# Kernel tuning notes

Measured on AMD Instinct MI355X. Metric: run time of the kernel, lower is better.

## Reference

```python
import jax, jax.numpy as jnp
import numpy as np

N_NODES = 50000
N_EDGES = 800000
IN_DIM = 128
ATT_DIM = 128
NEG_SLOPE = 0.01  # nn.LeakyReLU default


def setup_inputs() -> dict:
    key = jax.random.key(0)
    ks = jax.random.split(key, 8)
    x = jax.random.normal(ks[0], (N_NODES, IN_DIM), dtype=jnp.float32)
    src_idx = jax.random.randint(ks[1], (N_EDGES,), 0, N_NODES, dtype=jnp.int32)
    dst_idx = jax.random.randint(ks[2], (N_EDGES,), 0, N_NODES, dtype=jnp.int32)
    # small init scale keeps exp(score) numerically tame
    src_w = jax.random.normal(ks[3], (IN_DIM, ATT_DIM), dtype=jnp.float32) * 0.05
    src_b = jnp.zeros((ATT_DIM,), dtype=jnp.float32)
    dst_w = jax.random.normal(ks[4], (IN_DIM, ATT_DIM), dtype=jnp.float32) * 0.05
    dst_b = jnp.zeros((ATT_DIM,), dtype=jnp.float32)
    att_w = jax.random.normal(ks[5], (ATT_DIM, 1), dtype=jnp.float32) * 0.05
    att_b = jnp.zeros((1,), dtype=jnp.float32)
    return {"x": x, "src_idx": src_idx, "dst_idx": dst_idx,
            "src_w": src_w, "src_b": src_b, "dst_w": dst_w, "dst_b": dst_b,
            "att_w": att_w, "att_b": att_b}


def reference(x, src_idx, dst_idx, src_w, src_b, dst_w, dst_b, att_w, att_b):
    n = x.shape[0]
    # 1) mean aggregation of source features onto destinations (copy_u + mean)
    deg = jax.ops.segment_sum(jnp.ones_like(dst_idx, dtype=x.dtype), dst_idx, num_segments=n)
    h_mean = jax.ops.segment_sum(x[src_idx], dst_idx, num_segments=n)
    h_mean = h_mean / jnp.maximum(deg, 1.0)[:, None]
    # 2) attention projections on nodes (dense GEMMs)
    ha_src = x @ src_w + src_b          # [N, att_dim]
    ha_dst = h_mean @ dst_w + dst_b     # [N, att_dim]
    # 3) per-edge u_add_v -> LeakyReLU -> att Linear -> exp
    e = jax.nn.leaky_relu(ha_src[src_idx] + ha_dst[dst_idx], NEG_SLOPE)  # [E, att_dim]
    s = jnp.exp(e @ att_w + att_b)      # [E, 1]
    # 4) edge softmax: normalize by segment sum over destination
    denom = jax.ops.segment_sum(s, dst_idx, num_segments=n)  # [N, 1]
    a = s / denom[dst_idx]              # [E, 1]
    # 5) u_mul_e weighted aggregation (sum)
    out = jax.ops.segment_sum(x[src_idx] * a, dst_idx, num_segments=n)  # [N, in_dim]
    return out
```

## Files before the change

### kernel.cpp

```cpp
#include <hip/hip_runtime.h>
#include <math.h>

#define N_NODES 50000
#define N_EDGES 800000
#define DIM 128
#define NEG_SLOPE 0.01f
#define CAP 64
#define DEGS 32

#define GEMM_BLOCKS ((N_NODES + 63) / 64)
#define EPB 1024

typedef short v8s __attribute__((ext_vector_type(8)));
typedef float v4f __attribute__((ext_vector_type(4)));

__device__ inline unsigned f2bf2(float a, float b) {
    unsigned ua = __float_as_uint(a);
    unsigned ub = __float_as_uint(b);
    ua = (ua + 0x7fffu + ((ua >> 16) & 1u)) >> 16;
    ub = (ub + 0x7fffu + ((ub >> 16) & 1u)) & 0xffff0000u;
    return ua | ub;
}
__device__ inline float2 bf2f(unsigned u) {
    float2 r;
    r.x = __uint_as_float(u << 16);
    r.y = __uint_as_float(u & 0xffff0000u);
    return r;
}

__device__ inline float2 pka(float2 a, float2 b) {
    return make_float2(a.x + b.x, a.y + b.y);
}
__device__ inline float2 pkfma(float2 a, float2 b, float2 c) {
    return make_float2(fmaf(a.x, b.x, c.x), fmaf(a.y, b.y, c.y));
}
__device__ inline float2 leaky2(float2 v) {
    return make_float2(fmaxf(v.x, v.x * NEG_SLOPE), fmaxf(v.y, v.y * NEG_SLOPE));
}

#define ROR_ADD(v, CTRL) \
    ((v) + __int_as_float(__builtin_amdgcn_update_dpp( \
        0, __float_as_int(v), (CTRL), 0xf, 0xf, false)))

__global__ __launch_bounds__(256) void k_prepw(
    const float* __restrict__ src_w, const float* __restrict__ dst_w,
    unsigned* __restrict__ whT, int* __restrict__ deg)
{
    int gid = blockIdx.x * 256 + threadIdx.x;
    if (gid < 256 * 64) {
        int n = gid >> 6;
        int kk = gid & 63;
        const float* W = (n < 128) ? src_w : dst_w;
        int col = n & 127;
        float w0 = W[(2 * kk) * DIM + col];
        float w1 = W[(2 * kk + 1) * DIM + col];
        whT[gid] = f2bf2(w0, w1);
    }
    if (gid < N_NODES) deg[gid * DEGS] = 0;
}

__global__ __launch_bounds__(256) void k_scatgemm(
    const int* __restrict__ src, const int* __restrict__ dst,
    int* __restrict__ deg, int* __restrict__ slots,
    const float* __restrict__ x, const unsigned* __restrict__ whT,
    const float* __restrict__ src_b, unsigned* __restrict__ hx_u,
    unsigned* __restrict__ yu)
{
    __shared__ unsigned lds[4][16][132];
    int tid = threadIdx.x;
    int bx = blockIdx.x;

    int e0 = bx * EPB + tid;
    int sv[4], dv[4], pos[4];
    #pragma unroll
    for (int i = 0; i < 4; ++i) {
        int e = e0 + i * 256;
        bool v = (e < N_EDGES);
        sv[i] = v ? src[e] : 0;
        dv[i] = v ? dst[e] : 0;
    }
    #pragma unroll
    for (int i = 0; i < 4; ++i) {
        int e = e0 + i * 256;
        pos[i] = (e < N_EDGES) ? atomicAdd(&deg[dv[i] * DEGS], 1) : CAP;
    }

    int wave = tid >> 6;
    int lane = tid & 63;
    int quad = lane >> 4;
    int m = lane & 15;
    unsigned (*L)[132] = lds[wave];
    int rbase0 = bx * 64 + wave * 16;
    int arow = rbase0 + m;
    bool live = (arow < N_NODES);

    v8s b[4];
    #pragma unroll
    for (int k0 = 0; k0 < 4; ++k0) {
        float4 f0 = make_float4(0.f, 0.f, 0.f, 0.f);
        float4 f1 = f0;
        if (live) {
            const float4* xp = (const float4*)(x + (size_t)arow * DIM + k0 * 32 + quad * 8);
            f0 = xp[0];
            f1 = xp[1];
        }
        union { unsigned u[4]; v8s s; } pk;
        pk.u[0] = f2bf2(f0.x, f0.y);
        pk.u[1] = f2bf2(f0.z, f0.w);
        pk.u[2] = f2bf2(f1.x, f1.y);
        pk.u[3] = f2bf2(f1.z, f1.w);
        b[k0] = pk.s;
        int c = k0 * 32 + quad * 8 + 1;
        L[m][c + 0] = pk.u[0];
        L[m][c + 2] = pk.u[1];
        L[m][c + 4] = pk.u[2];
        L[m][c + 6] = pk.u[3];
    }

    #pragma unroll
    for (int i = 0; i < 4; ++i)
        if (pos[i] < CAP) slots[dv[i] * CAP + pos[i]] = sv[i] * 64;

    v4f yacc[8];
    #pragma unroll
    for (int nt = 0; nt < 16; ++nt) {
        v4f acc = {0.f, 0.f, 0.f, 0.f};
        const uint4* ap = (const uint4*)(whT + (size_t)(nt * 16 + m) * 64 + quad * 4);
        #pragma unroll
        for (int k0 = 0; k0 < 4; ++k0) {
            union { uint4 u; v8s s; } af;
            af.u = ap[k0 * 4];
            acc = __builtin_amdgcn_mfma_f32_16x16x32_bf16(af.s, b[k0], acc, 0, 0, 0);
        }
        if (nt < 8) {
            float4 bia = ((const float4*)src_b)[nt * 4 + quad];
            int c = nt * 16 + quad * 4;
            L[m][c]     = f2bf2(acc[0] + bia.x, acc[1] + bia.y);
            L[m][c + 2] = f2bf2(acc[2] + bia.z, acc[3] + bia.w);
        } else {
            yacc[nt - 8] = acc;
        }
    }

    for (int i = lane; i < 512; i += 64) {
        int r = i >> 5, c = i & 31;
        int row = rbase0 + r;
        if (row < N_NODES)
            ((uint4*)(hx_u + (size_t)row * 128))[c] = *(const uint4*)&L[r][c * 4];
    }

    #pragma unroll
    for (int t = 0; t < 8; ++t) {
        int c = t * 8 + quad * 2;
        L[m][c]     = f2bf2(yacc[t][0], yacc[t][1]);
        L[m][c + 1] = f2bf2(yacc[t][2], yacc[t][3]);
    }
    for (int i = lane; i < 256; i += 64) {
        int r = i >> 4, c = i & 15;
        int row = rbase0 + r;
        if (row < N_NODES)
            ((uint4*)(yu + (size_t)row * 64))[c] = *(const uint4*)&L[r][c * 4];
    }
}

__global__ __launch_bounds__(256) void k_fuse(
    const uint2* __restrict__ hx, const unsigned* __restrict__ yu,
    const int* __restrict__ slots, const int* __restrict__ deg,
    const float* __restrict__ dst_b, const float* __restrict__ att_w,
    const float* __restrict__ att_b, float* __restrict__ out)
{
    int g = blockIdx.x * 256 + threadIdx.x;
    int node = g >> 6;
    int lane = g & 63;
    int grp = lane >> 4;
    int sl = lane & 15;
    int cnt = deg[node * DEGS];
    if (cnt == 0) {
        if (grp < 2) {
            v4f z = {0.f, 0.f, 0.f, 0.f};
            __builtin_nontemporal_store(z, (v4f*)out + node * 32 + 2 * sl + grp);
        }
        return;
    }
    int cc = (cnt < CAP) ? cnt : CAP;
    int trips = (cc + 3) >> 2;
    int myoff = (lane < cc) ? slots[node * CAP + lane] : 0;

    float2 hd01 = {0.f, 0.f}, hd23 = {0.f, 0.f};
    float2 hd45 = {0.f, 0.f}, hd67 = {0.f, 0.f};
    #pragma unroll 2
    for (int t = 0; t < trips; ++t) {
        int i = 4 * t + grp;
        bool valid = (i < cc);
        int off = __shfl(myoff, valid ? i : 0);
        if (valid) {
            uint4 q = *((const uint4*)(yu + off) + sl);
            hd01 = pka(hd01, bf2f(q.x));
            hd23 = pka(hd23, bf2f(q.y));
            hd45 = pka(hd45, bf2f(q.z));
            hd67 = pka(hd67, bf2f(q.w));
        }
    }
    float inv = 1.0f / (float)cnt;
    float4 db0 = ((const float4*)dst_b)[2 * sl];
    float4 db1 = ((const float4*)dst_b)[2 * sl + 1];
    #define XRED(f) { f += __shfl_xor(f, 32); f += __shfl_xor(f, 16); f *= inv; }
    XRED(hd01.x) XRED(hd01.y) XRED(hd23.x) XRED(hd23.y)
    XRED(hd45.x) XRED(hd45.y) XRED(hd67.x) XRED(hd67.y)
    #undef XRED
    hd01.x += db0.x; hd01.y += db0.y; hd23.x += db0.z; hd23.y += db0.w;
    hd45.x += db1.x; hd45.y += db1.y; hd67.x += db1.z; hd67.y += db1.w;

    float4 aw0 = ((const float4*)att_w)[2 * sl];
    float4 aw1 = ((const float4*)att_w)[2 * sl + 1];
    float2 aw01 = make_float2(aw0.x, aw0.y), aw23 = make_float2(aw0.z, aw0.w);
    float2 aw45 = make_float2(aw1.x, aw1.y), aw67 = make_float2(aw1.z, aw1.w);
    float ab = att_b[0];
    float2 o01 = {0.f, 0.f}, o23 = {0.f, 0.f};
    float2 o45 = {0.f, 0.f}, o67 = {0.f, 0.f};
    float dsum = 0.f;
    #pragma unroll 2
    for (int t = 0; t < trips; ++t) {
        int i = 4 * t + grp;
        bool valid = (i < cc);
        int off = __shfl(myoff, valid ? i : 0);
        if (valid) {
            const uint4* hp = (const uint4*)(hx + off);
            uint4 qa = hp[2 * sl];
            uint4 qb = hp[2 * sl + 1];
            float2 p2 = {0.f, 0.f};
            p2 = pkfma(leaky2(pka(bf2f(qa.x), hd01)), aw01, p2);
            p2 = pkfma(leaky2(pka(bf2f(qa.z), hd23)), aw23, p2);
            p2 = pkfma(leaky2(pka(bf2f(qb.x), hd45)), aw45, p2);
            p2 = pkfma(leaky2(pka(bf2f(qb.z), hd67)), aw67, p2);
            float p = p2.x + p2.y;
            p = ROR_ADD(p, 0x128);
            p = ROR_ADD(p, 0x124);
            p = ROR_ADD(p, 0x122);
            p = ROR_ADD(p, 0x121);
            float s = __expf(p + ab);
            float2 s2 = make_float2(s, s);
            o01 = pkfma(bf2f(qa.y), s2, o01);
            o23 = pkfma(bf2f(qa.w), s2, o23);
            o45 = pkfma(bf2f(qb.y), s2, o45);
            o67 = pkfma(bf2f(qb.w), s2, o67);
            dsum += s;
        }
    }
    dsum += __shfl_xor(dsum, 32);
    dsum += __shfl_xor(dsum, 16);
    #define XRED2(f) { f += __shfl_xor(f, 32); f += __shfl_xor(f, 16); }
    XRED2(o01.x) XRED2(o01.y) XRED2(o23.x) XRED2(o23.y)
    XRED2(o45.x) XRED2(o45.y) XRED2(o67.x) XRED2(o67.y)
    #undef XRED2
    float r = 1.0f / dsum;
    if (grp < 2) {
        v4f ov;
        if (grp == 0) {
            ov[0] = o01.x * r; ov[1] = o01.y * r; ov[2] = o23.x * r; ov[3] = o23.y * r;
        } else {
            ov[0] = o45.x * r; ov[1] = o45.y * r; ov[2] = o67.x * r; ov[3] = o67.y * r;
        }
        __builtin_nontemporal_store(ov, (v4f*)out + node * 32 + 2 * sl + grp);
    }
}

extern "C" void kernel_launch(void* const* d_in, const int* in_sizes, int n_in,
                              void* d_out, int out_size, void* d_ws, size_t ws_size,
                              hipStream_t stream)
{
    const float* x     = (const float*)d_in[0];
    const int*   src   = (const int*)d_in[1];
    const int*   dst   = (const int*)d_in[2];
    const float* src_w = (const float*)d_in[3];
    const float* src_b = (const float*)d_in[4];
    const float* dst_w = (const float*)d_in[5];
    const float* dst_b = (const float*)d_in[6];
    const float* att_w = (const float*)d_in[7];
    const float* att_b = (const float*)d_in[8];
    float* out = (float*)d_out;
    (void)in_sizes; (void)n_in; (void)out_size; (void)ws_size;

    const size_t NF = (size_t)N_NODES * DIM;

    int* ws = (int*)d_ws;
    int* ideg  = ws;
    int* slots = ws + 1600512;
    unsigned* whT = (unsigned*)(ws + 4800512);
    unsigned* yu  = whT + 16384;
    uint2*    hx  = (uint2*)(yu + NF / 2);

    k_prepw<<<256, 256, 0, stream>>>(src_w, dst_w, whT, ideg);

    k_scatgemm<<<GEMM_BLOCKS, 256, 0, stream>>>(
        src, dst, ideg, slots, x, whT, src_b, (unsigned*)hx, yu);

    k_fuse<<<N_NODES * 64 / 256, 256, 0, stream>>>(
        hx, yu, slots, ideg, dst_b, att_w, att_b, out);
}
```

Before: 248.4 us.

## Split scatter-GEMM into single-wave blocks and defer edge atomics to the end

The fused scatter+GEMM kernel now launches 3125 one-wave blocks of 64 threads, each handling 16 node rows and 256 edges, instead of 782 four-wave blocks. All x loads and edge index loads are issued up front, and the degree atomics plus slot writes move to the end of the kernel so their latency overlaps the MFMA work. Bounds checks are dropped because both problem sizes divide evenly by the new tiling. The point is more independent waves to hide latency and less stalling on atomics, at the cost of hardcoding divisibility assumptions.

```diff
diff --git a/kernel.cpp b/kernel.cpp
--- a/kernel.cpp
+++ b/kernel.cpp
@@ -8,8 +8,7 @@
 #define CAP 64
 #define DEGS 32
 
-#define GEMM_BLOCKS ((N_NODES + 63) / 64)
-#define EPB 1024
+#define SG_BLOCKS 3125
 
 typedef short v8s __attribute__((ext_vector_type(8)));
 typedef float v4f __attribute__((ext_vector_type(4)));
@@ -59,56 +58,44 @@
     if (gid < N_NODES) deg[gid * DEGS] = 0;
 }
 
-__global__ __launch_bounds__(256) void k_scatgemm(
+__global__ __launch_bounds__(64, 4) void k_scatgemm(
     const int* __restrict__ src, const int* __restrict__ dst,
     int* __restrict__ deg, int* __restrict__ slots,
     const float* __restrict__ x, const unsigned* __restrict__ whT,
     const float* __restrict__ src_b, unsigned* __restrict__ hx_u,
     unsigned* __restrict__ yu)
 {
-    __shared__ unsigned lds[4][16][132];
-    int tid = threadIdx.x;
+    __shared__ unsigned L[16][132];
     int bx = blockIdx.x;
-
-    int e0 = bx * EPB + tid;
-    int sv[4], dv[4], pos[4];
-    #pragma unroll
-    for (int i = 0; i < 4; ++i) {
-        int e = e0 + i * 256;
-        bool v = (e < N_EDGES);
-        sv[i] = v ? src[e] : 0;
-        dv[i] = v ? dst[e] : 0;
-    }
-    #pragma unroll
-    for (int i = 0; i < 4; ++i) {
-        int e = e0 + i * 256;
-        pos[i] = (e < N_EDGES) ? atomicAdd(&deg[dv[i] * DEGS], 1) : CAP;
-    }
-
-    int wave = tid >> 6;
-    int lane = tid & 63;
+    int lane = threadIdx.x;
     int quad = lane >> 4;
     int m = lane & 15;
-    unsigned (*L)[132] = lds[wave];
-    int rbase0 = bx * 64 + wave * 16;
-    int arow = rbase0 + m;
-    bool live = (arow < N_NODES);
+
+    int arow = bx * 16 + m;
+    const float4* xp = (const float4*)(x + (size_t)arow * DIM + quad * 8);
+    float4 f[4][2];
+    #pragma unroll
+    for (int k0 = 0; k0 < 4; ++k0) {
+        f[k0][0] = xp[k0 * 8];
+        f[k0][1] = xp[k0 * 8 + 1];
+    }
+
+    int e0 = bx * 256 + lane;
+    int sv[4], dv[4];
+    #pragma unroll
+    for (int i = 0; i < 4; ++i) {
+        sv[i] = src[e0 + i * 64];
+        dv[i] = dst[e0 + i * 64];
+    }
 
     v8s b[4];
     #pragma unroll
     for (int k0 = 0; k0 < 4; ++k0) {
-        float4 f0 = make_float4(0.f, 0.f, 0.f, 0.f);
-        float4 f1 = f0;
-        if (live) {
-            const float4* xp = (const float4*)(x + (size_t)arow * DIM + k0 * 32 + quad * 8);
-            f0 = xp[0];
-            f1 = xp[1];
-        }
         union { unsigned u[4]; v8s s; } pk;
-        pk.u[0] = f2bf2(f0.x, f0.y);
-        pk.u[1] = f2bf2(f0.z, f0.w);
-        pk.u[2] = f2bf2(f1.x, f1.y);
-        pk.u[3] = f2bf2(f1.z, f1.w);
+        pk.u[0] = f2bf2(f[k0][0].x, f[k0][0].y);
+        pk.u[1] = f2bf2(f[k0][0].z, f[k0][0].w);
+        pk.u[2] = f2bf2(f[k0][1].x, f[k0][1].y);
+        pk.u[3] = f2bf2(f[k0][1].z, f[k0][1].w);
         b[k0] = pk.s;
         int c = k0 * 32 + quad * 8 + 1;
         L[m][c + 0] = pk.u[0];
@@ -116,10 +103,6 @@
         L[m][c + 4] = pk.u[2];
         L[m][c + 6] = pk.u[3];
     }
-
-    #pragma unroll
-    for (int i = 0; i < 4; ++i)
-        if (pos[i] < CAP) slots[dv[i] * CAP + pos[i]] = sv[i] * 64;
 
     v4f yacc[8];
     #pragma unroll
@@ -142,11 +125,10 @@
         }
     }
 
+    int rbase0 = bx * 16;
     for (int i = lane; i < 512; i += 64) {
         int r = i >> 5, c = i & 31;
-        int row = rbase0 + r;
-        if (row < N_NODES)
-            ((uint4*)(hx_u + (size_t)row * 128))[c] = *(const uint4*)&L[r][c * 4];
+        ((uint4*)(hx_u + (size_t)(rbase0 + r) * 128))[c] = *(const uint4*)&L[r][c * 4];
     }
 
     #pragma unroll
@@ -157,10 +139,16 @@
     }
     for (int i = lane; i < 256; i += 64) {
         int r = i >> 4, c = i & 15;
-        int row = rbase0 + r;
-        if (row < N_NODES)
-            ((uint4*)(yu + (size_t)row * 64))[c] = *(const uint4*)&L[r][c * 4];
-    }
+        ((uint4*)(yu + (size_t)(rbase0 + r) * 64))[c] = *(const uint4*)&L[r][c * 4];
+    }
+
+    int pos[4];
+    #pragma unroll
+    for (int i = 0; i < 4; ++i)
+        pos[i] = atomicAdd(&deg[dv[i] * DEGS], 1);
+    #pragma unroll
+    for (int i = 0; i < 4; ++i)
+        if (pos[i] < CAP) slots[dv[i] * CAP + pos[i]] = sv[i] * 64;
 }
 
 __global__ __launch_bounds__(256) void k_fuse(
@@ -292,7 +280,7 @@
 
     k_prepw<<<256, 256, 0, stream>>>(src_w, dst_w, whT, ideg);
 
-    k_scatgemm<<<GEMM_BLOCKS, 256, 0, stream>>>(
+    k_scatgemm<<<SG_BLOCKS, 64, 0, stream>>>(
         src, dst, ideg, slots, x, whT, src_b, (unsigned*)hx, yu);
 
     k_fuse<<<N_NODES * 64 / 256, 256, 0, stream>>>(
```

Result: no change. 252.6 us (+1.7%).
